# Kernel optimization log

Hardware: AMD Instinct MI355X
Metric: run time of the kernel (lower is better)

Reference implementation:

```python
import jax, jax.numpy as jnp
import numpy as np

# blocks, d_model, heads, ffn_hidden, vocab, gen_len=(image_size//4)**2
L, D, NH, FF, V, GEN = 4, 256, 8, 1024, 2048, 16
B, NS, SLOT = 8, 7, 256  # batch, num_slots+1 (slots + projected action), slot_size


def setup_inputs():
    key = jax.random.key(0)
    ks = jax.random.split(key, 16)
    def n(i, shape, s=0.02):
        return (jax.random.normal(ks[i], shape) * s).astype(jnp.float32)
    return dict(
        slots=jax.random.normal(ks[0], (B, NS, SLOT), dtype=jnp.float32),
        W_slot_proj=n(1, (SLOT, D)),
        dict_emb=n(2, (V + 1, D)),
        pe=n(3, (GEN + 1, D)),
        ln_self_w=jnp.ones((L, D)), ln_self_b=jnp.zeros((L, D)),
        Wq_s=n(4, (L, D, D)), Wk_s=n(5, (L, D, D)), Wv_s=n(6, (L, D, D)), Wo_s=n(7, (L, D, D)),
        ln_cross_w=jnp.ones((L, D)), ln_cross_b=jnp.zeros((L, D)),
        Wq_c=n(8, (L, D, D)), Wk_c=n(9, (L, D, D)), Wv_c=n(10, (L, D, D)), Wo_c=n(11, (L, D, D)),
        ln_ffn_w=jnp.ones((L, D)), ln_ffn_b=jnp.zeros((L, D)),
        W1=n(12, (L, D, FF)), b1=jnp.zeros((L, FF)),
        W2=n(13, (L, FF, D)), b2=jnp.zeros((L, D)),
        ln_f_w=jnp.ones((D,)), ln_f_b=jnp.zeros((D,)),
        W_out=n(14, (D, V)),
    )


def _ln(x, w, b, eps=1e-5):
    m = x.mean(-1, keepdims=True)
    v = ((x - m) ** 2).mean(-1, keepdims=True)
    return (x - m) * jax.lax.rsqrt(v + eps) * w + b


def _mha(q_in, k_in, v_in, Wq, Wk, Wv, Wo, mask=None):
    Bq, Tq, Dm = q_in.shape
    dh = Dm // NH
    q = (q_in @ Wq).reshape(Bq, Tq, NH, dh).transpose(0, 2, 1, 3) * (dh ** -0.5)
    k = (k_in @ Wk).reshape(Bq, -1, NH, dh).transpose(0, 2, 1, 3)
    v = (v_in @ Wv).reshape(Bq, -1, NH, dh).transpose(0, 2, 1, 3)
    att = jnp.einsum('bhqd,bhkd->bhqk', q, k)
    if mask is not None:
        att = att + mask
    att = jax.nn.softmax(att, axis=-1)
    o = jnp.einsum('bhqk,bhkd->bhqd', att, v)
    return o.transpose(0, 2, 1, 3).reshape(Bq, Tq, Dm) @ Wo


def _decoder(x, enc, P):
    T = x.shape[1]
    i = jnp.arange(T)
    mask = jnp.where(i[:, None] >= i[None, :], 0.0, -jnp.inf).astype(x.dtype)
    for l in range(L):
        h = _ln(x, P['ln_self_w'][l], P['ln_self_b'][l])
        if l == 0:
            x = h  # SLATE: first block normalizes residual stream in-place
        x = x + _mha(h, h, h, P['Wq_s'][l], P['Wk_s'][l], P['Wv_s'][l], P['Wo_s'][l], mask)
        h = _ln(x, P['ln_cross_w'][l], P['ln_cross_b'][l])
        x = x + _mha(h, enc, enc, P['Wq_c'][l], P['Wk_c'][l], P['Wv_c'][l], P['Wo_c'][l])
        h = _ln(x, P['ln_ffn_w'][l], P['ln_ffn_b'][l])
        x = x + (jax.nn.relu(h @ P['W1'][l] + P['b1'][l]) @ P['W2'][l] + P['b2'][l])
    return _ln(x, P['ln_f_w'], P['ln_f_b'])


def _slots2tokens(slots, W_slot_proj, dict_emb, pe, P, W_out):
    Bb = slots.shape[0]
    enc = slots @ W_slot_proj  # slot_proj (bias=False)
    Tf = GEN + 1
    # fixed-size token buffer; position 0 is BOS one-hot, future slots are zeros
    # (causal mask guarantees they never influence position t's output)
    buf = jnp.zeros((Bb, Tf, V + 1), jnp.float32).at[:, 0, 0].set(1.0)

    def step(buf, t):
        tok = jnp.argmax(buf, axis=-1)              # [B, Tf]
        emb = dict_emb[tok] + pe[None, :Tf]         # OneHotDictionary + PositionalEncoding
        dec = _decoder(emb, enc, P)
        logits_t = dec[:, t] @ W_out                # [B, V]
        z_next = jax.nn.one_hot(jnp.argmax(logits_t, -1), V, dtype=buf.dtype)
        upd = jnp.pad(z_next, ((0, 0), (1, 0)))[:, None, :]  # prepend BOS column
        buf = jax.lax.dynamic_update_slice(buf, upd, (0, t + 1, 0))
        return buf, (z_next, logits_t)

    _, (z_gen, logits) = jax.lax.scan(step, buf, jnp.arange(GEN))
    z_gen = jnp.moveaxis(z_gen, 0, 1)    # [B, GEN, V]
    logits = jnp.moveaxis(logits, 0, 1)  # [B, GEN, V]
    He = int(np.sqrt(GEN))               # H_enc = W_enc = image_size // 4
    z_img = z_gen.transpose(0, 2, 1).reshape(Bb, V, He, He)
    return z_img, jax.nn.log_softmax(logits, axis=-1)


def reference(slots, W_slot_proj, dict_emb, pe, ln_self_w, ln_self_b, Wq_s, Wk_s, Wv_s, Wo_s, ln_cross_w, ln_cross_b, Wq_c, Wk_c, Wv_c, Wo_c, ln_ffn_w, ln_ffn_b, W1, b1, W2, b2, ln_f_w, ln_f_b, W_out):
    P = dict(ln_self_w=ln_self_w, ln_self_b=ln_self_b, Wq_s=Wq_s, Wk_s=Wk_s, Wv_s=Wv_s, Wo_s=Wo_s,
             ln_cross_w=ln_cross_w, ln_cross_b=ln_cross_b, Wq_c=Wq_c, Wk_c=Wk_c, Wv_c=Wv_c, Wo_c=Wo_c,
             ln_ffn_w=ln_ffn_w, ln_ffn_b=ln_ffn_b, W1=W1, b1=b1, W2=W2, b2=b2,
             ln_f_w=ln_f_w, ln_f_b=ln_f_b)
    return _slots2tokens(slots, W_slot_proj, dict_emb, pe, P, W_out)
```

## Files before the change

### kernel.cpp

```cpp
#include <hip/hip_runtime.h>

#define D       256
#define DH      32
#define FFDIM   1024
#define VOCAB   2048
#define GENLEN  16
#define BATCH   8
#define NSLOT   7
#define TF      17
#define NLAYER  4

#define SCOPE_AGENT __HIP_MEMORY_SCOPE_AGENT

typedef float    f32x4 __attribute__((ext_vector_type(4)));
typedef unsigned u32x4 __attribute__((ext_vector_type(4)));

struct Params {
  const float *slots, *W_slot_proj, *dict_emb, *pe;
  const float *ln_self_w, *ln_self_b, *Wq_s, *Wk_s, *Wv_s, *Wo_s;
  const float *ln_cross_w, *ln_cross_b, *Wq_c, *Wk_c, *Wv_c, *Wo_c;
  const float *ln_ffn_w, *ln_ffn_b, *W1, *b1, *W2, *b2;
  const float *ln_f_w, *ln_f_b, *W_out;
  float *enc, *P0, *P1, *tri;
  unsigned *flags;
  float *out_z, *out_lp;
};

__device__ __forceinline__ float cload(const float* p) {
  return __hip_atomic_load(p, __ATOMIC_RELAXED, SCOPE_AGENT);
}
__device__ __forceinline__ void cstore(float* p, float v) {
  __hip_atomic_store(p, v, __ATOMIC_RELAXED, SCOPE_AGENT);
}

__device__ __forceinline__ float blockSum(float v, float* red) {
  #pragma unroll
  for (int o = 32; o > 0; o >>= 1) v += __shfl_down(v, o);
  const int lane = threadIdx.x & 63, w = threadIdx.x >> 6;
  if (lane == 0) red[w] = v;
  __syncthreads();
  float s = red[0] + red[1] + red[2] + red[3];
  __syncthreads();
  return s;
}

template<int N>
__device__ __forceinline__ float dotStreamPre(const float* __restrict__ W,
                                              const float* __restrict__ h,
                                              int i0, int ld,
                                              const float* __restrict__ pre) {
  float pA[32], pB[32];
  #pragma unroll
  for (int k = 0; k < 32; ++k) pA[k] = pre[k];
  #pragma unroll
  for (int k = 0; k < 32; ++k) pB[k] = W[(size_t)(i0 + 32 + k) * ld];
  float acc = 0.f;
  #pragma unroll 1
  for (int u = 0; u < N; u += 64) {
    const f32x4* h4 = reinterpret_cast<const f32x4*>(h + i0 + u);
    #pragma unroll
    for (int k = 0; k < 8; ++k) {
      const f32x4 hv = h4[k];
      acc = fmaf(hv.x, pA[4*k+0], acc); acc = fmaf(hv.y, pA[4*k+1], acc);
      acc = fmaf(hv.z, pA[4*k+2], acc); acc = fmaf(hv.w, pA[4*k+3], acc);
    }
    if (u + 64 < N) {
      #pragma unroll
      for (int k = 0; k < 32; ++k) pA[k] = W[(size_t)(i0 + u + 64 + k) * ld];
    }
    #pragma unroll
    for (int k = 0; k < 8; ++k) {
      const f32x4 hv = h4[8 + k];
      acc = fmaf(hv.x, pB[4*k+0], acc); acc = fmaf(hv.y, pB[4*k+1], acc);
      acc = fmaf(hv.z, pB[4*k+2], acc); acc = fmaf(hv.w, pB[4*k+3], acc);
    }
    if (u + 96 < N) {
      #pragma unroll
      for (int k = 0; k < 32; ++k) pB[k] = W[(size_t)(i0 + u + 96 + k) * ld];
    }
  }
  return acc;
}

template<int N>
__device__ __forceinline__ float dotStream(const float* __restrict__ W,
                                           const float* __restrict__ h,
                                           int i0, int ld) {
  float pre[32];
  #pragma unroll
  for (int k = 0; k < 32; ++k) pre[k] = W[(size_t)(i0 + k) * ld];
  return dotStreamPre<N>(W, h, i0, ld, pre);
}

__device__ __forceinline__ float dot32(const float* __restrict__ w,
                                       const float* __restrict__ h, int i0) {
  float acc = 0.f;
  const f32x4* h4 = reinterpret_cast<const f32x4*>(h + i0);
  #pragma unroll
  for (int k = 0; k < 8; ++k) {
    const f32x4 hv = h4[k];
    acc = fmaf(hv.x, w[4*k+0], acc); acc = fmaf(hv.y, w[4*k+1], acc);
    acc = fmaf(hv.z, w[4*k+2], acc); acc = fmaf(hv.w, w[4*k+3], acc);
  }
  return acc;
}

__global__ __launch_bounds__(256, 1) void mega_kernel(Params p)
{
  const int blk = blockIdx.x;
  const int bb = blk >> 3, sl = blk & 7, tid = threadIdx.x;
  unsigned* flags = p.flags + bb * 256;
  unsigned target = 0;

  __shared__ __align__(16) float hsh[D];
  __shared__ __align__(16) float ash[128];
  __shared__ float qsh[DH], osh[DH], score[TF], red[4];
  __shared__ float wval[4]; __shared__ int widx[4];
  __shared__ float stage[NSLOT * D];
  __shared__ float kls[NLAYER][TF][DH + 1], vls[NLAYER][TF][DH + 1];
  __shared__ float kcls[NLAYER][NSLOT][DH + 1], vcls[NLAYER][NSLOT][DH + 1];

  auto gsync = [&]() {
    __syncthreads();
    ++target;
    if (tid == 0)
      __hip_atomic_store(flags + sl, target, __ATOMIC_RELAXED, SCOPE_AGENT);
  };
  auto gwait = [&]() {
    u32x4 f0, f1;
    for (;;) {
      asm volatile(
        "global_load_dwordx4 %0, %2, off sc0 sc1\n\t"
        "global_load_dwordx4 %1, %2, off offset:16 sc0 sc1\n\t"
        "s_waitcnt vmcnt(0)"
        : "=&v"(f0), "=&v"(f1) : "v"(flags) : "memory");
      if (f0.x >= target && f0.y >= target && f0.z >= target && f0.w >= target &&
          f1.x >= target && f1.y >= target && f1.z >= target && f1.w >= target)
        break;
      __builtin_amdgcn_s_sleep(1);
    }
  };

  auto layernorm = [&](float xv, const float* w, const float* b) -> float {
    const float mean = blockSum(xv, red) * (1.f / D);
    const float dv = xv - mean;
    const float var = blockSum(dv * dv, red) * (1.f / D);
    return dv * (1.f / sqrtf(var + 1e-5f)) * w[tid] + b[tid];
  };

  auto fold8 = [&](const float* P) -> float {
    const float* a0 = P + (bb * 8 + 0) * D + tid;
    const float* a4 = P + (bb * 8 + 4) * D + tid;
    float s0, s1, s2, s3, s4, s5, s6, s7;
    asm volatile(
      "global_load_dword %0, %8, off sc0 sc1\n\t"
      "global_load_dword %1, %8, off offset:1024 sc0 sc1\n\t"
      "global_load_dword %2, %8, off offset:2048 sc0 sc1\n\t"
      "global_load_dword %3, %8, off offset:3072 sc0 sc1\n\t"
      "global_load_dword %4, %9, off sc0 sc1\n\t"
      "global_load_dword %5, %9, off offset:1024 sc0 sc1\n\t"
      "global_load_dword %6, %9, off offset:2048 sc0 sc1\n\t"
      "global_load_dword %7, %9, off offset:3072 sc0 sc1\n\t"
      "s_waitcnt vmcnt(0)"
      : "=&v"(s0), "=&v"(s1), "=&v"(s2), "=&v"(s3),
        "=&v"(s4), "=&v"(s5), "=&v"(s6), "=&v"(s7)
      : "v"(a0), "v"(a4));
    return ((s0 + s1) + (s2 + s3)) + ((s4 + s5) + (s6 + s7));
  };

  float heldLogit = 0.f;
  int   lastAmax  = 0;

  auto consume_tri = [&](int row) {
    const float* tb = p.tri + bb * 64;
    f32x4 q0,q1,q2,q3,q4,q5,q6,q7;
    asm volatile(
      "global_load_dwordx4 %0, %8, off sc0 sc1\n\t"
      "global_load_dwordx4 %1, %8, off offset:32 sc0 sc1\n\t"
      "global_load_dwordx4 %2, %8, off offset:64 sc0 sc1\n\t"
      "global_load_dwordx4 %3, %8, off offset:96 sc0 sc1\n\t"
      "global_load_dwordx4 %4, %8, off offset:128 sc0 sc1\n\t"
      "global_load_dwordx4 %5, %8, off offset:160 sc0 sc1\n\t"
      "global_load_dwordx4 %6, %8, off offset:192 sc0 sc1\n\t"
      "global_load_dwordx4 %7, %8, off offset:224 sc0 sc1\n\t"
      "s_waitcnt vmcnt(0)"
      : "=&v"(q0), "=&v"(q1), "=&v"(q2), "=&v"(q3),
        "=&v"(q4), "=&v"(q5), "=&v"(q6), "=&v"(q7)
      : "v"(tb));
    float gm = q0.x;
    gm = fmaxf(gm, q1.x); gm = fmaxf(gm, q2.x); gm = fmaxf(gm, q3.x);
    gm = fmaxf(gm, q4.x); gm = fmaxf(gm, q5.x); gm = fmaxf(gm, q6.x); gm = fmaxf(gm, q7.x);
    float gs = 0.f; float best = -1e30f; int am = 0;
    const f32x4 qa[8] = {q0,q1,q2,q3,q4,q5,q6,q7};
    #pragma unroll
    for (int j = 0; j < 8; ++j) {
      gs += qa[j].y * expf(qa[j].x - gm);
      if (qa[j].x > best) { best = qa[j].x; am = j * 256 + (int)qa[j].z; }
    }
    const float lse = gm + logf(gs);
    p.out_lp[(bb * GENLEN + row) * VOCAB + sl * 256 + tid] = heldLogit - lse;
    if (sl == 0 && tid == 0)
      p.out_z[bb * VOCAB * GENLEN + am * GENLEN + row] = 1.0f;
    lastAmax = am;
  };

  for (int i = tid; i < NLAYER * TF * (DH + 1); i += 256) {
    (&kls[0][0][0])[i] = 0.f;
    (&vls[0][0][0])[i] = 0.f;
  }

  if (tid < 32) {
    const int c = sl * 32 + tid;
    float acc[NSLOT] = {0.f,0.f,0.f,0.f,0.f,0.f,0.f};
    #pragma unroll 8
    for (int i = 0; i < D; ++i) {
      const float w = p.W_slot_proj[i * D + c];
      #pragma unroll
      for (int s = 0; s < NSLOT; ++s) acc[s] += p.slots[(bb * NSLOT + s) * D + i] * w;
    }
    for (int s = 0; s < NSLOT; ++s) cstore(&p.enc[(bb * NSLOT + s) * D + c], acc[s]);
  }
  gsync(); gwait();

  {
    for (int i = tid; i < NSLOT * D; i += 256) stage[i] = cload(&p.enc[bb * NSLOT * D + i]);
    __syncthreads();
    const int l = tid >> 6, g = tid & 63, c32 = g >> 1, mat = g & 1;
    const float* W = (mat ? p.Wv_c : p.Wk_c) + l * D * D + sl * DH + c32;
    float acc[NSLOT] = {0.f,0.f,0.f,0.f,0.f,0.f,0.f};
    #pragma unroll 8
    for (int i = 0; i < D; ++i) {
      const float w = W[i * D];
      #pragma unroll
      for (int s = 0; s < NSLOT; ++s) acc[s] += stage[s * D + i] * w;
    }
    if (mat) { for (int s = 0; s < NSLOT; ++s) vcls[l][s][c32] = acc[s]; }
    else     { for (int s = 0; s < NSLOT; ++s) kcls[l][s][c32] = acc[s]; }
    __syncthreads();
  }

  float* Pbuf[2] = {p.P0, p.P1};
  int par = 0;
  float x = 0.f;

  #pragma unroll 1
  for (int t = 0; t < GENLEN; ++t) {
    #pragma unroll 1
    for (int l = 0; l < NLAYER; ++l) {
      {
        gsync();
        const int mm = tid >> 6, g = tid & 63, c32 = g >> 1, half = g & 1;
        const float* Wqkv = (mm == 0 ? p.Wq_s : (mm == 1 ? p.Wk_s : p.Wv_s))
                          + l * D * D + sl * DH + c32;
        float preq[32];
        if (tid < 192) {
          #pragma unroll
          for (int k = 0; k < 32; ++k) preq[k] = Wqkv[(size_t)(half * 128 + k) * D];
        }
        float wo[32];
        {
          const float* W = p.Wo_s + l * D * D + sl * DH * D + tid;
          #pragma unroll
          for (int k = 0; k < 32; ++k) wo[k] = W[(size_t)k * D];
        }
        gwait();

        if (l == 0) {
          int tok = 0;
          if (t > 0) { consume_tri(t - 1); tok = lastAmax + 1; }
          x = p.dict_emb[tok * D + tid] + p.pe[t * D + tid];
        } else {
          x += fold8(Pbuf[par]);
        }
        const float h = layernorm(x, p.ln_self_w + l * D, p.ln_self_b + l * D);
        if (l == 0) x = h;
        hsh[tid] = h;
        __syncthreads();

        if (tid < 192) {
          float acc = dotStreamPre<128>(Wqkv, hsh, half * 128, D, preq);
          acc += __shfl_xor(acc, 1);
          if (half == 0) {
            if (mm == 0)      qsh[c32] = acc * 0.17677669529663689f;
            else if (mm == 1) kls[l][t][c32] = acc;
            else              vls[l][t][c32] = acc;
          }
        }
        __syncthreads();

        if (tid < 64) {
          float s = -1e30f;
          if (tid <= t) {
            float a = 0.f;
            #pragma unroll
            for (int r = 0; r < DH; ++r) a += qsh[r] * kls[l][tid][r];
            s = a;
          }
          float m = s;
          #pragma unroll
          for (int o = 32; o > 0; o >>= 1) m = fmaxf(m, __shfl_xor(m, o));
          const float e = (tid <= t) ? expf(s - m) : 0.f;
          float sum = e;
          #pragma unroll
          for (int o = 32; o > 0; o >>= 1) sum += __shfl_xor(sum, o);
          const float inv = 1.f / sum;
          if (tid < TF) score[tid] = e * inv;
        }
        __syncthreads();
        if (tid < DH) {
          float a = 0.f;
          #pragma unroll
          for (int pp = 0; pp < TF; ++pp) a = fmaf(score[pp], vls[l][pp][tid], a);
          osh[tid] = a;
        }
        __syncthreads();
        {
          float a0 = 0.f;
          #pragma unroll
          for (int k = 0; k < 32; ++k) a0 = fmaf(osh[k], wo[k], a0);
          cstore(&Pbuf[par ^ 1][(bb * 8 + sl) * D + tid], a0);
        }
        par ^= 1;
      }

      {
        gsync();
        const int c32 = tid >> 3, sub = tid & 7;
        float wq[32], woc[32];
        {
          const float* W = p.Wq_c + l * D * D + sl * DH + c32;
          #pragma unroll
          for (int k = 0; k < 32; ++k) wq[k] = W[(size_t)(sub * 32 + k) * D];
        }
        {
          const float* W = p.Wo_c + l * D * D + sl * DH * D + tid;
          #pragma unroll
          for (int k = 0; k < 32; ++k) woc[k] = W[(size_t)k * D];
        }
        gwait();

        x += fold8(Pbuf[par]);
        hsh[tid] = layernorm(x, p.ln_cross_w + l * D, p.ln_cross_b + l * D);
        __syncthreads();

        {
          float acc = dot32(wq, hsh, sub * 32);
          acc += __shfl_xor(acc, 1);
          acc += __shfl_xor(acc, 2);
          acc += __shfl_xor(acc, 4);
          if (sub == 0) qsh[c32] = acc * 0.17677669529663689f;
        }
        __syncthreads();

        if (tid < 64) {
          float s = -1e30f;
          if (tid < NSLOT) {
            float a = 0.f;
            #pragma unroll
            for (int r = 0; r < DH; ++r) a += qsh[r] * kcls[l][tid][r];
            s = a;
          }
          float m = s;
          #pragma unroll
          for (int o = 32; o > 0; o >>= 1) m = fmaxf(m, __shfl_xor(m, o));
          const float e = (tid < NSLOT) ? expf(s - m) : 0.f;
          float sum = e;
          #pragma unroll
          for (int o = 32; o > 0; o >>= 1) sum += __shfl_xor(sum, o);
          const float inv = 1.f / sum;
          if (tid < NSLOT) score[tid] = e * inv;
        }
        __syncthreads();
        if (tid < DH) {
          float a = 0.f;
          #pragma unroll
          for (int s = 0; s < NSLOT; ++s) a = fmaf(score[s], vcls[l][s][tid], a);
          osh[tid] = a;
        }
        __syncthreads();
        {
          float a0 = 0.f;
          #pragma unroll
          for (int k = 0; k < 32; ++k) a0 = fmaf(osh[k], woc[k], a0);
          cstore(&Pbuf[par ^ 1][(bb * 8 + sl) * D + tid], a0);
        }
        par ^= 1;
      }

      {
        gsync();
        const int c128 = tid >> 1, half = tid & 1, c = sl * 128 + c128;
        const float* W1p = p.W1 + l * D * FFDIM + c;
        float prew1[32];
        {
          #pragma unroll
          for (int k = 0; k < 32; ++k) prew1[k] = W1p[(size_t)(half * 128 + k) * FFDIM];
        }
        gwait();

        x += fold8(Pbuf[par]);
        hsh[tid] = layernorm(x, p.ln_ffn_w + l * D, p.ln_ffn_b + l * D);
        __syncthreads();

        {
          float acc = dotStreamPre<128>(W1p, hsh, half * 128, FFDIM, prew1);
          acc += __shfl_xor(acc, 1);
          if (half == 0) ash[c128] = fmaxf(acc + p.b1[l * FFDIM + c], 0.f);
        }
        __syncthreads();
        {
          float acc = dotStream<128>(p.W2 + l * FFDIM * D + sl * 128 * D + tid, ash, 0, D);
          if (sl == 0) acc += p.b2[l * D + tid];
          cstore(&Pbuf[par ^ 1][(bb * 8 + sl) * D + tid], acc);
        }
        __syncthreads();
      }
      par ^= 1;
    }

    {
      gsync();
      const float* Wop = p.W_out + sl * 256 + tid;
      float prewo[32];
      {
        #pragma unroll
        for (int k = 0; k < 32; ++k) prewo[k] = Wop[(size_t)k * VOCAB];
      }
      gwait();

      x += fold8(Pbuf[par]);
      hsh[tid] = layernorm(x, p.ln_f_w, p.ln_f_b);
      __syncthreads();
      heldLogit = dotStreamPre<256>(Wop, hsh, 0, VOCAB, prewo);

      {
        float v = heldLogit; int idx = tid;
        #pragma unroll
        for (int o = 32; o > 0; o >>= 1) {
          const float v2 = __shfl_xor(v, o);
          const int   i2 = __shfl_xor(idx, o);
          if (v2 > v || (v2 == v && i2 < idx)) { v = v2; idx = i2; }
        }
        const int w = tid >> 6;
        if ((tid & 63) == 0) { wval[w] = v; widx[w] = idx; }
      }
      __syncthreads();
      float smax = wval[0]; int sarg = widx[0];
      #pragma unroll
      for (int j = 1; j < 4; ++j)
        if (wval[j] > smax || (wval[j] == smax && widx[j] < sarg)) { smax = wval[j]; sarg = widx[j]; }
      const float ssum = blockSum(expf(heldLogit - smax), red);
      if (tid == 0) {
        cstore(&p.tri[(bb * 8 + sl) * 8 + 0], smax);
        cstore(&p.tri[(bb * 8 + sl) * 8 + 1], ssum);
        cstore(&p.tri[(bb * 8 + sl) * 8 + 2], (float)sarg);
      }
      __syncthreads();
    }
  }

  gsync(); gwait();
  consume_tri(GENLEN - 1);
}

extern "C" void kernel_launch(void* const* d_in, const int* in_sizes, int n_in,
                              void* d_out, int out_size, void* d_ws, size_t ws_size,
                              hipStream_t stream)
{
  Params p;
  const float* const* in = (const float* const*)d_in;
  p.slots = in[0];  p.W_slot_proj = in[1]; p.dict_emb = in[2]; p.pe = in[3];
  p.ln_self_w = in[4];  p.ln_self_b = in[5];
  p.Wq_s = in[6];  p.Wk_s = in[7];  p.Wv_s = in[8];  p.Wo_s = in[9];
  p.ln_cross_w = in[10]; p.ln_cross_b = in[11];
  p.Wq_c = in[12]; p.Wk_c = in[13]; p.Wv_c = in[14]; p.Wo_c = in[15];
  p.ln_ffn_w = in[16]; p.ln_ffn_b = in[17];
  p.W1 = in[18]; p.b1 = in[19]; p.W2 = in[20]; p.b2 = in[21];
  p.ln_f_w = in[22]; p.ln_f_b = in[23]; p.W_out = in[24];

  p.flags = (unsigned*)d_ws;
  float* ws = (float*)d_ws + BATCH * 256;
  p.enc = ws;  ws += BATCH * NSLOT * D;
  p.P0  = ws;  ws += BATCH * 8 * D;
  p.P1  = ws;  ws += BATCH * 8 * D;
  p.tri = ws;  ws += BATCH * 8 * 8;

  p.out_z  = (float*)d_out;
  p.out_lp = (float*)d_out + BATCH * VOCAB * GENLEN;

  hipMemsetAsync(d_ws, 0, BATCH * 256 * sizeof(unsigned), stream);
  hipMemsetAsync(d_out, 0, (size_t)out_size * sizeof(float), stream);

  mega_kernel<<<64, 256, 0, stream>>>(p);
}
```

Before: 1.463 ms.

## Stage per-layer weight tiles into LDS via async global-to-LDS loads

Weight slices for self-attention QKV/O, cross-attention Q/O, the FFN W2 block and the first half of W_out are issued as `__builtin_amdgcn_global_load_lds` copies into a 128KB shared buffer before the grid-wide flag wait. The matvecs then read weights from LDS instead of from register prefetch arrays. The aim is to overlap more weight fetch with the inter-block barrier and to cut register pressure from large prefetch arrays. The trade-offs are heavy LDS occupancy, possible bank conflicts on strided LDS reads, and completion of the async copies now relying on the waitcnt inside the wait routine plus a block sync.

```diff
diff --git a/kernel.cpp b/kernel.cpp
--- a/kernel.cpp
+++ b/kernel.cpp
@@ -82,41 +82,19 @@
   return acc;
 }
 
-template<int N>
-__device__ __forceinline__ float dotStream(const float* __restrict__ W,
-                                           const float* __restrict__ h,
-                                           int i0, int ld) {
-  float pre[32];
-  #pragma unroll
-  for (int k = 0; k < 32; ++k) pre[k] = W[(size_t)(i0 + k) * ld];
-  return dotStreamPre<N>(W, h, i0, ld, pre);
-}
-
-__device__ __forceinline__ float dot32(const float* __restrict__ w,
-                                       const float* __restrict__ h, int i0) {
-  float acc = 0.f;
-  const f32x4* h4 = reinterpret_cast<const f32x4*>(h + i0);
-  #pragma unroll
-  for (int k = 0; k < 8; ++k) {
-    const f32x4 hv = h4[k];
-    acc = fmaf(hv.x, w[4*k+0], acc); acc = fmaf(hv.y, w[4*k+1], acc);
-    acc = fmaf(hv.z, w[4*k+2], acc); acc = fmaf(hv.w, w[4*k+3], acc);
-  }
-  return acc;
-}
-
 __global__ __launch_bounds__(256, 1) void mega_kernel(Params p)
 {
   const int blk = blockIdx.x;
   const int bb = blk >> 3, sl = blk & 7, tid = threadIdx.x;
+  const int wv = tid >> 6, la = tid & 63;
   unsigned* flags = p.flags + bb * 256;
   unsigned target = 0;
 
+  __shared__ __align__(16) float wbuf[32768];
   __shared__ __align__(16) float hsh[D];
   __shared__ __align__(16) float ash[128];
   __shared__ float qsh[DH], osh[DH], score[TF], red[4];
   __shared__ float wval[4]; __shared__ int widx[4];
-  __shared__ float stage[NSLOT * D];
   __shared__ float kls[NLAYER][TF][DH + 1], vls[NLAYER][TF][DH + 1];
   __shared__ float kcls[NLAYER][NSLOT][DH + 1], vcls[NLAYER][NSLOT][DH + 1];
 
@@ -223,7 +201,7 @@
   gsync(); gwait();
 
   {
-    for (int i = tid; i < NSLOT * D; i += 256) stage[i] = cload(&p.enc[bb * NSLOT * D + i]);
+    for (int i = tid; i < NSLOT * D; i += 256) wbuf[i] = cload(&p.enc[bb * NSLOT * D + i]);
     __syncthreads();
     const int l = tid >> 6, g = tid & 63, c32 = g >> 1, mat = g & 1;
     const float* W = (mat ? p.Wv_c : p.Wk_c) + l * D * D + sl * DH + c32;
@@ -232,7 +210,7 @@
     for (int i = 0; i < D; ++i) {
       const float w = W[i * D];
       #pragma unroll
-      for (int s = 0; s < NSLOT; ++s) acc[s] += stage[s * D + i] * w;
+      for (int s = 0; s < NSLOT; ++s) acc[s] += wbuf[s * D + i] * w;
     }
     if (mat) { for (int s = 0; s < NSLOT; ++s) vcls[l][s][c32] = acc[s]; }
     else     { for (int s = 0; s < NSLOT; ++s) kcls[l][s][c32] = acc[s]; }
@@ -249,19 +227,20 @@
     for (int l = 0; l < NLAYER; ++l) {
       {
         gsync();
-        const int mm = tid >> 6, g = tid & 63, c32 = g >> 1, half = g & 1;
-        const float* Wqkv = (mm == 0 ? p.Wq_s : (mm == 1 ? p.Wk_s : p.Wv_s))
-                          + l * D * D + sl * DH + c32;
-        float preq[32];
-        if (tid < 192) {
-          #pragma unroll
-          for (int k = 0; k < 32; ++k) preq[k] = Wqkv[(size_t)(half * 128 + k) * D];
-        }
-        float wo[32];
-        {
-          const float* W = p.Wo_s + l * D * D + sl * DH * D + tid;
-          #pragma unroll
-          for (int k = 0; k < 32; ++k) wo[k] = W[(size_t)k * D];
+        {
+          const float* qb = p.Wq_s + l * D * D;
+          const float* kb = p.Wk_s + l * D * D;
+          const float* vb = p.Wv_s + l * D * D;
+          for (int j = wv; j < 96; j += 4) {
+            const int m = j >> 5, jj = j & 31;
+            const float* mb = (m == 0) ? qb : (m == 1) ? kb : vb;
+            const float* src = mb + (jj * 8 + (la >> 3)) * D + sl * 32 + (la & 7) * 4;
+            __builtin_amdgcn_global_load_lds(src, &wbuf[m * 8192 + jj * 256], 16, 0, 0);
+          }
+          const float* ob = p.Wo_s + l * D * D + sl * 32 * D;
+          for (int j = wv; j < 32; j += 4)
+            __builtin_amdgcn_global_load_lds(ob + j * 256 + la * 4,
+                                             &wbuf[24576 + j * 256], 16, 0, 0);
         }
         gwait();
 
@@ -278,7 +257,12 @@
         __syncthreads();
 
         if (tid < 192) {
-          float acc = dotStreamPre<128>(Wqkv, hsh, half * 128, D, preq);
+          const int mm = tid >> 6, g = tid & 63, c32 = g >> 1, half = g & 1;
+          const int wb = mm * 8192 + c32;
+          float acc = 0.f;
+          #pragma unroll 8
+          for (int k = 0; k < 128; ++k)
+            acc = fmaf(hsh[half * 128 + k], wbuf[wb + (half * 128 + k) * 32], acc);
           acc += __shfl_xor(acc, 1);
           if (half == 0) {
             if (mm == 0)      qsh[c32] = acc * 0.17677669529663689f;
@@ -317,7 +301,7 @@
         {
           float a0 = 0.f;
           #pragma unroll
-          for (int k = 0; k < 32; ++k) a0 = fmaf(osh[k], wo[k], a0);
+          for (int k = 0; k < 32; ++k) a0 = fmaf(osh[k], wbuf[24576 + k * 256 + tid], a0);
           cstore(&Pbuf[par ^ 1][(bb * 8 + sl) * D + tid], a0);
         }
         par ^= 1;
@@ -325,17 +309,16 @@
 
       {
         gsync();
-        const int c32 = tid >> 3, sub = tid & 7;
-        float wq[32], woc[32];
-        {
-          const float* W = p.Wq_c + l * D * D + sl * DH + c32;
-          #pragma unroll
-          for (int k = 0; k < 32; ++k) wq[k] = W[(size_t)(sub * 32 + k) * D];
-        }
-        {
-          const float* W = p.Wo_c + l * D * D + sl * DH * D + tid;
-          #pragma unroll
-          for (int k = 0; k < 32; ++k) woc[k] = W[(size_t)k * D];
+        {
+          const float* qb = p.Wq_c + l * D * D;
+          for (int j = wv; j < 32; j += 4) {
+            const float* src = qb + (j * 8 + (la >> 3)) * D + sl * 32 + (la & 7) * 4;
+            __builtin_amdgcn_global_load_lds(src, &wbuf[j * 256], 16, 0, 0);
+          }
+          const float* ob = p.Wo_c + l * D * D + sl * 32 * D;
+          for (int j = wv; j < 32; j += 4)
+            __builtin_amdgcn_global_load_lds(ob + j * 256 + la * 4,
+                                             &wbuf[8192 + j * 256], 16, 0, 0);
         }
         gwait();
 
@@ -344,7 +327,11 @@
         __syncthreads();
 
         {
-          float acc = dot32(wq, hsh, sub * 32);
+          const int c32 = tid >> 3, sub = tid & 7;
+          float acc = 0.f;
+          #pragma unroll
+          for (int k = 0; k < 32; ++k)
+            acc = fmaf(hsh[sub * 32 + k], wbuf[(sub * 32 + k) * 32 + c32], acc);
           acc += __shfl_xor(acc, 1);
           acc += __shfl_xor(acc, 2);
           acc += __shfl_xor(acc, 4);
@@ -381,7 +368,7 @@
         {
           float a0 = 0.f;
           #pragma unroll
-          for (int k = 0; k < 32; ++k) a0 = fmaf(osh[k], woc[k], a0);
+          for (int k = 0; k < 32; ++k) a0 = fmaf(osh[k], wbuf[8192 + k * 256 + tid], a0);
           cstore(&Pbuf[par ^ 1][(bb * 8 + sl) * D + tid], a0);
         }
         par ^= 1;
@@ -389,6 +376,12 @@
 
       {
         gsync();
+        {
+          const float* w2b = p.W2 + l * FFDIM * D + sl * 128 * D;
+          for (int j = wv; j < 128; j += 4)
+            __builtin_amdgcn_global_load_lds(w2b + j * 256 + la * 4,
+                                             &wbuf[j * 256], 16, 0, 0);
+        }
         const int c128 = tid >> 1, half = tid & 1, c = sl * 128 + c128;
         const float* W1p = p.W1 + l * D * FFDIM + c;
         float prew1[32];
@@ -409,7 +402,9 @@
         }
         __syncthreads();
         {
-          float acc = dotStream<128>(p.W2 + l * FFDIM * D + sl * 128 * D + tid, ash, 0, D);
+          float acc = 0.f;
+          #pragma unroll 8
+          for (int r = 0; r < 128; ++r) acc = fmaf(ash[r], wbuf[r * 256 + tid], acc);
           if (sl == 0) acc += p.b2[l * D + tid];
           cstore(&Pbuf[par ^ 1][(bb * 8 + sl) * D + tid], acc);
         }
@@ -420,18 +415,43 @@
 
     {
       gsync();
+      {
+        for (int j = wv; j < 128; j += 4) {
+          const float* src = p.W_out + j * VOCAB + sl * 256 + la * 4;
+          __builtin_amdgcn_global_load_lds(src, &wbuf[j * 256], 16, 0, 0);
+        }
+      }
       const float* Wop = p.W_out + sl * 256 + tid;
-      float prewo[32];
+      float pD[32];
       {
         #pragma unroll
-        for (int k = 0; k < 32; ++k) prewo[k] = Wop[(size_t)k * VOCAB];
+        for (int k = 0; k < 32; ++k) pD[k] = Wop[(size_t)(128 + k) * VOCAB];
       }
       gwait();
 
       x += fold8(Pbuf[par]);
       hsh[tid] = layernorm(x, p.ln_f_w, p.ln_f_b);
       __syncthreads();
-      heldLogit = dotStreamPre<256>(Wop, hsh, 0, VOCAB, prewo);
+
+      float acc = 0.f;
+      #pragma unroll 8
+      for (int r = 0; r < 128; ++r) acc = fmaf(hsh[r], wbuf[r * 256 + tid], acc);
+      float pE[32];
+      #pragma unroll
+      for (int k = 0; k < 32; ++k) pE[k] = Wop[(size_t)(160 + k) * VOCAB];
+      #pragma unroll
+      for (int k = 0; k < 32; ++k) acc = fmaf(hsh[128 + k], pD[k], acc);
+      #pragma unroll
+      for (int k = 0; k < 32; ++k) pD[k] = Wop[(size_t)(192 + k) * VOCAB];
+      #pragma unroll
+      for (int k = 0; k < 32; ++k) acc = fmaf(hsh[160 + k], pE[k], acc);
+      #pragma unroll
+      for (int k = 0; k < 32; ++k) pE[k] = Wop[(size_t)(224 + k) * VOCAB];
+      #pragma unroll
+      for (int k = 0; k < 32; ++k) acc = fmaf(hsh[192 + k], pD[k], acc);
+      #pragma unroll
+      for (int k = 0; k < 32; ++k) acc = fmaf(hsh[224 + k], pE[k], acc);
+      heldLogit = acc;
 
       {
         float v = heldLogit; int idx = tid;
@@ -441,8 +461,7 @@
           const int   i2 = __shfl_xor(idx, o);
           if (v2 > v || (v2 == v && i2 < idx)) { v = v2; idx = i2; }
         }
-        const int w = tid >> 6;
-        if ((tid & 63) == 0) { wval[w] = v; widx[w] = idx; }
+        if ((tid & 63) == 0) { wval[wv] = v; widx[wv] = idx; }
       }
       __syncthreads();
       float smax = wval[0]; int sarg = widx[0];
```

Measured after the change: 1.974 ms. 1.35x slower.

## Double block size to 512 threads and split dot products across more lanes

Applied to the files above, without the earlier changes.

Raises the persistent megakernel from 256 to 512 threads per block. QKV, W1, W2 and W_out matrix-vector products now split their reduction dimension over more lanes, with shuffle reductions combining the partial sums. W2 weights are also prefetched before the grid wait. The goal is more memory-level parallelism on the latency-bound decode steps, at the cost of more block-wide reduction and sync overhead, and some threads sit idle in the LN and attention phases.

```diff
diff --git a/kernel.cpp b/kernel.cpp
--- a/kernel.cpp
+++ b/kernel.cpp
@@ -9,6 +9,7 @@
 #define NSLOT   7
 #define TF      17
 #define NLAYER  4
+#define NT      512
 
 #define SCOPE_AGENT __HIP_MEMORY_SCOPE_AGENT
 
@@ -39,7 +40,8 @@
   const int lane = threadIdx.x & 63, w = threadIdx.x >> 6;
   if (lane == 0) red[w] = v;
   __syncthreads();
-  float s = red[0] + red[1] + red[2] + red[3];
+  float s = ((red[0] + red[1]) + (red[2] + red[3])) +
+            ((red[4] + red[5]) + (red[6] + red[7]));
   __syncthreads();
   return s;
 }
@@ -82,39 +84,18 @@
   return acc;
 }
 
-template<int N>
-__device__ __forceinline__ float dotStream(const float* __restrict__ W,
-                                           const float* __restrict__ h,
-                                           int i0, int ld) {
-  float pre[32];
-  #pragma unroll
-  for (int k = 0; k < 32; ++k) pre[k] = W[(size_t)(i0 + k) * ld];
-  return dotStreamPre<N>(W, h, i0, ld, pre);
-}
-
-__device__ __forceinline__ float dot32(const float* __restrict__ w,
-                                       const float* __restrict__ h, int i0) {
-  float acc = 0.f;
-  const f32x4* h4 = reinterpret_cast<const f32x4*>(h + i0);
-  #pragma unroll
-  for (int k = 0; k < 8; ++k) {
-    const f32x4 hv = h4[k];
-    acc = fmaf(hv.x, w[4*k+0], acc); acc = fmaf(hv.y, w[4*k+1], acc);
-    acc = fmaf(hv.z, w[4*k+2], acc); acc = fmaf(hv.w, w[4*k+3], acc);
-  }
-  return acc;
-}
-
-__global__ __launch_bounds__(256, 1) void mega_kernel(Params p)
+__global__ __launch_bounds__(NT, 1) void mega_kernel(Params p)
 {
   const int blk = blockIdx.x;
   const int bb = blk >> 3, sl = blk & 7, tid = threadIdx.x;
+  const int wv = tid >> 6;
   unsigned* flags = p.flags + bb * 256;
   unsigned target = 0;
 
   __shared__ __align__(16) float hsh[D];
   __shared__ __align__(16) float ash[128];
-  __shared__ float qsh[DH], osh[DH], score[TF], red[4];
+  __shared__ __align__(16) float lg[256];
+  __shared__ float qsh[DH], osh[DH], score[TF], red[8];
   __shared__ float wval[4]; __shared__ int widx[4];
   __shared__ float stage[NSLOT * D];
   __shared__ float kls[NLAYER][TF][DH + 1], vls[NLAYER][TF][DH + 1];
@@ -144,8 +125,10 @@
   auto layernorm = [&](float xv, const float* w, const float* b) -> float {
     const float mean = blockSum(xv, red) * (1.f / D);
     const float dv = xv - mean;
-    const float var = blockSum(dv * dv, red) * (1.f / D);
-    return dv * (1.f / sqrtf(var + 1e-5f)) * w[tid] + b[tid];
+    const float var = blockSum((tid < 256) ? dv * dv : 0.f, red) * (1.f / D);
+    float r = 0.f;
+    if (tid < 256) r = dv * (1.f / sqrtf(var + 1e-5f)) * w[tid] + b[tid];
+    return r;
   };
 
   auto fold8 = [&](const float* P) -> float {
@@ -204,7 +187,7 @@
     lastAmax = am;
   };
 
-  for (int i = tid; i < NLAYER * TF * (DH + 1); i += 256) {
+  for (int i = tid; i < NLAYER * TF * (DH + 1); i += NT) {
     (&kls[0][0][0])[i] = 0.f;
     (&vls[0][0][0])[i] = 0.f;
   }
@@ -223,19 +206,21 @@
   gsync(); gwait();
 
   {
-    for (int i = tid; i < NSLOT * D; i += 256) stage[i] = cload(&p.enc[bb * NSLOT * D + i]);
+    for (int i = tid; i < NSLOT * D; i += NT) stage[i] = cload(&p.enc[bb * NSLOT * D + i]);
     __syncthreads();
-    const int l = tid >> 6, g = tid & 63, c32 = g >> 1, mat = g & 1;
-    const float* W = (mat ? p.Wv_c : p.Wk_c) + l * D * D + sl * DH + c32;
-    float acc[NSLOT] = {0.f,0.f,0.f,0.f,0.f,0.f,0.f};
-    #pragma unroll 8
-    for (int i = 0; i < D; ++i) {
-      const float w = W[i * D];
-      #pragma unroll
-      for (int s = 0; s < NSLOT; ++s) acc[s] += stage[s * D + i] * w;
-    }
-    if (mat) { for (int s = 0; s < NSLOT; ++s) vcls[l][s][c32] = acc[s]; }
-    else     { for (int s = 0; s < NSLOT; ++s) kcls[l][s][c32] = acc[s]; }
+    if (tid < 256) {
+      const int l = tid >> 6, g = tid & 63, c32 = g >> 1, mat = g & 1;
+      const float* W = (mat ? p.Wv_c : p.Wk_c) + l * D * D + sl * DH + c32;
+      float acc[NSLOT] = {0.f,0.f,0.f,0.f,0.f,0.f,0.f};
+      #pragma unroll 8
+      for (int i = 0; i < D; ++i) {
+        const float w = W[i * D];
+        #pragma unroll
+        for (int s = 0; s < NSLOT; ++s) acc[s] += stage[s * D + i] * w;
+      }
+      if (mat) { for (int s = 0; s < NSLOT; ++s) vcls[l][s][c32] = acc[s]; }
+      else     { for (int s = 0; s < NSLOT; ++s) kcls[l][s][c32] = acc[s]; }
+    }
     __syncthreads();
   }
 
@@ -249,38 +234,44 @@
     for (int l = 0; l < NLAYER; ++l) {
       {
         gsync();
-        const int mm = tid >> 6, g = tid & 63, c32 = g >> 1, half = g & 1;
+        const int mm = tid >> 7, r = tid & 127, c32 = r >> 2, q4 = r & 3;
         const float* Wqkv = (mm == 0 ? p.Wq_s : (mm == 1 ? p.Wk_s : p.Wv_s))
                           + l * D * D + sl * DH + c32;
         float preq[32];
-        if (tid < 192) {
-          #pragma unroll
-          for (int k = 0; k < 32; ++k) preq[k] = Wqkv[(size_t)(half * 128 + k) * D];
+        if (tid < 384) {
+          #pragma unroll
+          for (int k = 0; k < 32; ++k) preq[k] = Wqkv[(size_t)(q4 * 64 + k) * D];
         }
         float wo[32];
-        {
+        if (tid < 256) {
           const float* W = p.Wo_s + l * D * D + sl * DH * D + tid;
           #pragma unroll
           for (int k = 0; k < 32; ++k) wo[k] = W[(size_t)k * D];
         }
         gwait();
 
-        if (l == 0) {
-          int tok = 0;
-          if (t > 0) { consume_tri(t - 1); tok = lastAmax + 1; }
-          x = p.dict_emb[tok * D + tid] + p.pe[t * D + tid];
-        } else {
-          x += fold8(Pbuf[par]);
-        }
-        const float h = layernorm(x, p.ln_self_w + l * D, p.ln_self_b + l * D);
-        if (l == 0) x = h;
-        hsh[tid] = h;
-        __syncthreads();
-
-        if (tid < 192) {
-          float acc = dotStreamPre<128>(Wqkv, hsh, half * 128, D, preq);
+        float xv = 0.f;
+        if (tid < 256) {
+          if (l == 0) {
+            int tok = 0;
+            if (t > 0) { consume_tri(t - 1); tok = lastAmax + 1; }
+            xv = p.dict_emb[tok * D + tid] + p.pe[t * D + tid];
+          } else {
+            xv = x + fold8(Pbuf[par]);
+          }
+        }
+        const float h = layernorm(xv, p.ln_self_w + l * D, p.ln_self_b + l * D);
+        if (tid < 256) {
+          x = (l == 0) ? h : xv;
+          hsh[tid] = h;
+        }
+        __syncthreads();
+
+        if (tid < 384) {
+          float acc = dotStreamPre<64>(Wqkv, hsh, q4 * 64, D, preq);
           acc += __shfl_xor(acc, 1);
-          if (half == 0) {
+          acc += __shfl_xor(acc, 2);
+          if (q4 == 0) {
             if (mm == 0)      qsh[c32] = acc * 0.17677669529663689f;
             else if (mm == 1) kls[l][t][c32] = acc;
             else              vls[l][t][c32] = acc;
@@ -293,7 +284,7 @@
           if (tid <= t) {
             float a = 0.f;
             #pragma unroll
-            for (int r = 0; r < DH; ++r) a += qsh[r] * kls[l][tid][r];
+            for (int rr = 0; rr < DH; ++rr) a += qsh[rr] * kls[l][tid][rr];
             s = a;
           }
           float m = s;
@@ -314,7 +305,7 @@
           osh[tid] = a;
         }
         __syncthreads();
-        {
+        if (tid < 256) {
           float a0 = 0.f;
           #pragma unroll
           for (int k = 0; k < 32; ++k) a0 = fmaf(osh[k], wo[k], a0);
@@ -327,24 +318,31 @@
         gsync();
         const int c32 = tid >> 3, sub = tid & 7;
         float wq[32], woc[32];
-        {
+        if (tid < 256) {
           const float* W = p.Wq_c + l * D * D + sl * DH + c32;
           #pragma unroll
           for (int k = 0; k < 32; ++k) wq[k] = W[(size_t)(sub * 32 + k) * D];
-        }
-        {
-          const float* W = p.Wo_c + l * D * D + sl * DH * D + tid;
-          #pragma unroll
-          for (int k = 0; k < 32; ++k) woc[k] = W[(size_t)k * D];
+          const float* W2 = p.Wo_c + l * D * D + sl * DH * D + tid;
+          #pragma unroll
+          for (int k = 0; k < 32; ++k) woc[k] = W2[(size_t)k * D];
         }
         gwait();
 
-        x += fold8(Pbuf[par]);
-        hsh[tid] = layernorm(x, p.ln_cross_w + l * D, p.ln_cross_b + l * D);
-        __syncthreads();
-
-        {
-          float acc = dot32(wq, hsh, sub * 32);
+        float xv = 0.f;
+        if (tid < 256) xv = x + fold8(Pbuf[par]);
+        const float h = layernorm(xv, p.ln_cross_w + l * D, p.ln_cross_b + l * D);
+        if (tid < 256) { x = xv; hsh[tid] = h; }
+        __syncthreads();
+
+        if (tid < 256) {
+          float acc = 0.f;
+          const f32x4* h4 = reinterpret_cast<const f32x4*>(hsh + sub * 32);
+          #pragma unroll
+          for (int k = 0; k < 8; ++k) {
+            const f32x4 hv = h4[k];
+            acc = fmaf(hv.x, wq[4*k+0], acc); acc = fmaf(hv.y, wq[4*k+1], acc);
+            acc = fmaf(hv.z, wq[4*k+2], acc); acc = fmaf(hv.w, wq[4*k+3], acc);
+          }
           acc += __shfl_xor(acc, 1);
           acc += __shfl_xor(acc, 2);
           acc += __shfl_xor(acc, 4);
@@ -357,7 +355,7 @@
           if (tid < NSLOT) {
             float a = 0.f;
             #pragma unroll
-            for (int r = 0; r < DH; ++r) a += qsh[r] * kcls[l][tid][r];
+            for (int rr = 0; rr < DH; ++rr) a += qsh[rr] * kcls[l][tid][rr];
             s = a;
           }
           float m = s;
@@ -378,7 +376,7 @@
           osh[tid] = a;
         }
         __syncthreads();
-        {
+        if (tid < 256) {
           float a0 = 0.f;
           #pragma unroll
           for (int k = 0; k < 32; ++k) a0 = fmaf(osh[k], woc[k], a0);
@@ -389,29 +387,42 @@
 
       {
         gsync();
-        const int c128 = tid >> 1, half = tid & 1, c = sl * 128 + c128;
+        const int c128 = tid >> 2, q4 = tid & 3, c = sl * 128 + c128;
         const float* W1p = p.W1 + l * D * FFDIM + c;
         float prew1[32];
         {
           #pragma unroll
-          for (int k = 0; k < 32; ++k) prew1[k] = W1p[(size_t)(half * 128 + k) * FFDIM];
+          for (int k = 0; k < 32; ++k) prew1[k] = W1p[(size_t)(q4 * 64 + k) * FFDIM];
+        }
+        const int c2 = tid >> 1, hf = tid & 1;
+        const float* W2p = p.W2 + l * FFDIM * D + sl * 128 * D + c2;
+        float prew2[32];
+        {
+          #pragma unroll
+          for (int k = 0; k < 32; ++k) prew2[k] = W2p[(size_t)(hf * 64 + k) * D];
         }
         gwait();
 
-        x += fold8(Pbuf[par]);
-        hsh[tid] = layernorm(x, p.ln_ffn_w + l * D, p.ln_ffn_b + l * D);
+        float xv = 0.f;
+        if (tid < 256) xv = x + fold8(Pbuf[par]);
+        const float h = layernorm(xv, p.ln_ffn_w + l * D, p.ln_ffn_b + l * D);
+        if (tid < 256) { x = xv; hsh[tid] = h; }
         __syncthreads();
 
         {
-          float acc = dotStreamPre<128>(W1p, hsh, half * 128, FFDIM, prew1);
+          float acc = dotStreamPre<64>(W1p, hsh, q4 * 64, FFDIM, prew1);
           acc += __shfl_xor(acc, 1);
-          if (half == 0) ash[c128] = fmaxf(acc + p.b1[l * FFDIM + c], 0.f);
+          acc += __shfl_xor(acc, 2);
+          if (q4 == 0) ash[c128] = fmaxf(acc + p.b1[l * FFDIM + c], 0.f);
         }
         __syncthreads();
         {
-          float acc = dotStream<128>(p.W2 + l * FFDIM * D + sl * 128 * D + tid, ash, 0, D);
-          if (sl == 0) acc += p.b2[l * D + tid];
-          cstore(&Pbuf[par ^ 1][(bb * 8 + sl) * D + tid], acc);
+          float acc = dotStreamPre<64>(W2p, ash, hf * 64, D, prew2);
+          acc += __shfl_xor(acc, 1);
+          if (hf == 0) {
+            if (sl == 0) acc += p.b2[l * D + c2];
+            cstore(&Pbuf[par ^ 1][(bb * 8 + sl) * D + c2], acc);
+          }
         }
         __syncthreads();
       }
@@ -420,20 +431,30 @@
 
     {
       gsync();
-      const float* Wop = p.W_out + sl * 256 + tid;
+      const int j = tid >> 1, hf = tid & 1;
+      const float* Wop = p.W_out + sl * 256 + j;
       float prewo[32];
       {
         #pragma unroll
-        for (int k = 0; k < 32; ++k) prewo[k] = Wop[(size_t)k * VOCAB];
+        for (int k = 0; k < 32; ++k) prewo[k] = Wop[(size_t)(hf * 128 + k) * VOCAB];
       }
       gwait();
 
-      x += fold8(Pbuf[par]);
-      hsh[tid] = layernorm(x, p.ln_f_w, p.ln_f_b);
+      float xv = 0.f;
+      if (tid < 256) xv = x + fold8(Pbuf[par]);
+      const float h = layernorm(xv, p.ln_f_w, p.ln_f_b);
+      if (tid < 256) hsh[tid] = h;
       __syncthreads();
-      heldLogit = dotStreamPre<256>(Wop, hsh, 0, VOCAB, prewo);
 
       {
+        float acc = dotStreamPre<128>(Wop, hsh, hf * 128, VOCAB, prewo);
+        acc += __shfl_xor(acc, 1);
+        if (hf == 0) lg[j] = acc;
+      }
+      __syncthreads();
+      if (tid < 256) heldLogit = lg[tid];
+
+      if (tid < 256) {
         float v = heldLogit; int idx = tid;
         #pragma unroll
         for (int o = 32; o > 0; o >>= 1) {
@@ -441,15 +462,14 @@
           const int   i2 = __shfl_xor(idx, o);
           if (v2 > v || (v2 == v && i2 < idx)) { v = v2; idx = i2; }
         }
-        const int w = tid >> 6;
-        if ((tid & 63) == 0) { wval[w] = v; widx[w] = idx; }
+        if ((tid & 63) == 0) { wval[wv] = v; widx[wv] = idx; }
       }
       __syncthreads();
       float smax = wval[0]; int sarg = widx[0];
       #pragma unroll
-      for (int j = 1; j < 4; ++j)
-        if (wval[j] > smax || (wval[j] == smax && widx[j] < sarg)) { smax = wval[j]; sarg = widx[j]; }
-      const float ssum = blockSum(expf(heldLogit - smax), red);
+      for (int jj = 1; jj < 4; ++jj)
+        if (wval[jj] > smax || (wval[jj] == smax && widx[jj] < sarg)) { smax = wval[jj]; sarg = widx[jj]; }
+      const float ssum = blockSum((tid < 256) ? expf(heldLogit - smax) : 0.f, red);
       if (tid == 0) {
         cstore(&p.tri[(bb * 8 + sl) * 8 + 0], smax);
         cstore(&p.tri[(bb * 8 + sl) * 8 + 1], ssum);
@@ -460,7 +480,7 @@
   }
 
   gsync(); gwait();
-  consume_tri(GENLEN - 1);
+  if (tid < 256) consume_tri(GENLEN - 1);
 }
 
 extern "C" void kernel_launch(void* const* d_in, const int* in_sizes, int n_in,
@@ -491,5 +511,5 @@
   hipMemsetAsync(d_ws, 0, BATCH * 256 * sizeof(unsigned), stream);
   hipMemsetAsync(d_out, 0, (size_t)out_size * sizeof(float), stream);
 
-  mega_kernel<<<64, 256, 0, stream>>>(p);
+  mega_kernel<<<64, NT, 0, stream>>>(p);
 }
```

After: 3.064 ms. +109.5%, slower.
